# Kernel tuning notes

Hardware: AMD Instinct MI355X
Metric: run time of the kernel (lower is better)

Reference implementation:

```python
import jax, jax.numpy as jnp
from jax import lax
import numpy as np

B, L, C_IN, HID, RANK, NC = 256, 1024, 16, 512, 128, 10
PAD, K = 4, 7  # each conv block: L -> L + 2*PAD - K + 1 = L + 2


def _block(x, dwk, dwb, pwk, pwb, g, b):
    # x: (B, C, L); depthwise conv (groups=C) -> pointwise 1x1 -> batchnorm (batch stats) -> relu
    cin = dwk.shape[0]
    dn = ('NCH', 'OIH', 'NCH')
    y = lax.conv_general_dilated(x, dwk, (1,), [(PAD, PAD)], dimension_numbers=dn,
                                 feature_group_count=cin) + dwb[None, :, None]
    y = lax.conv_general_dilated(y, pwk, (1,), [(0, 0)], dimension_numbers=dn) + pwb[None, :, None]
    m = y.mean(axis=(0, 2), keepdims=True)
    v = y.var(axis=(0, 2), keepdims=True)
    y = (y - m) * lax.rsqrt(v + 1e-5) * g[None, :, None] + b[None, :, None]
    return jax.nn.relu(y)


def _cell(xp, h, c, Ui, Vi, Uh, Vh, bi, bh):
    # low-rank LSTM cell: W = U @ V kept factored for efficiency (same math)
    gates = (xp @ Ui) @ Vi + bi + (h @ Uh) @ Vh + bh  # (B, 4H)
    i, f, g, o = jnp.split(gates, 4, axis=1)
    c = jax.nn.sigmoid(f) * c + jax.nn.sigmoid(i) * jnp.tanh(g)
    h = jax.nn.sigmoid(o) * jnp.tanh(c)
    return h, c


def _forward(x, dw_k1, dw_b1, pw_k1, pw_b1, bn_g1, bn_b1,
             dw_k2, dw_b2, pw_k2, pw_b2, bn_g2, bn_b2,
             dw_k3, dw_b3, pw_k3, pw_b3, bn_g3, bn_b3,
             dw_k4, dw_b4, pw_k4, pw_b4, bn_g4, bn_b4,
             Ui1, Vi1, Uh1, Vh1, bi1, bh1,
             Ui2, Vi2, Uh2, Vh2, bi2, bh2,
             fc_w, fc_b):
    y = x[:, 0].transpose(0, 2, 1)  # (B, C_IN, L)
    y = _block(y, dw_k1, dw_b1, pw_k1, pw_b1, bn_g1, bn_b1)
    y = _block(y, dw_k2, dw_b2, pw_k2, pw_b2, bn_g2, bn_b2)
    y = _block(y, dw_k3, dw_b3, pw_k3, pw_b3, bn_g3, bn_b3)
    y = _block(y, dw_k4, dw_b4, pw_k4, pw_b4, bn_g4, bn_b4)
    # dropout = identity (eval)
    xs = y.transpose(2, 0, 1)  # (T, B, 32), T = L + 8
    bsz = xs.shape[1]
    z = jnp.zeros((bsz, HID), xs.dtype)

    def step(carry, xt):
        h1, c1, h2, c2 = carry
        h1, c1 = _cell(xt, h1, c1, Ui1, Vi1, Uh1, Vh1, bi1, bh1)
        h2, c2 = _cell(h1, h2, c2, Ui2, Vi2, Uh2, Vh2, bi2, bh2)
        return (h1, c1, h2, c2), None

    (h1, c1, h2, c2), _ = lax.scan(step, (z, z, z, z), xs)
    # original stacks all h2 then takes [:, -1, :] -> final h2; dropout = identity
    return h2 @ fc_w.T + fc_b  # (B, NC)


def setup_inputs() -> dict:
    key = jax.random.key(0)
    ks = iter(jax.random.split(key, 64))

    def n(shape, scale=0.05):
        return jax.random.normal(next(ks), shape, jnp.float32) * scale

    inp = {'x': jax.random.normal(next(ks), (B, 1, L, C_IN), jnp.float32)}
    chans = [C_IN, 32, 32, 32]
    for i, cin in enumerate(chans, start=1):
        inp[f'dw_k{i}'] = n((cin, 1, K))
        inp[f'dw_b{i}'] = jnp.zeros((cin,), jnp.float32)
        inp[f'pw_k{i}'] = n((32, cin, 1))
        inp[f'pw_b{i}'] = jnp.zeros((32,), jnp.float32)
        inp[f'bn_g{i}'] = jnp.ones((32,), jnp.float32)
        inp[f'bn_b{i}'] = jnp.zeros((32,), jnp.float32)
    inp['Ui1'] = n((32, RANK)); inp['Vi1'] = n((RANK, 4 * HID))
    inp['Uh1'] = n((HID, RANK)); inp['Vh1'] = n((RANK, 4 * HID))
    inp['bi1'] = jnp.zeros((4 * HID,), jnp.float32); inp['bh1'] = jnp.zeros((4 * HID,), jnp.float32)
    inp['Ui2'] = n((HID, RANK)); inp['Vi2'] = n((RANK, 4 * HID))
    inp['Uh2'] = n((HID, RANK)); inp['Vh2'] = n((RANK, 4 * HID))
    inp['bi2'] = jnp.zeros((4 * HID,), jnp.float32); inp['bh2'] = jnp.zeros((4 * HID,), jnp.float32)
    inp['fc_w'] = n((NC, HID)); inp['fc_b'] = jnp.zeros((NC,), jnp.float32)
    return inp


def reference(x, dw_k1, dw_b1, pw_k1, pw_b1, bn_g1, bn_b1,
              dw_k2, dw_b2, pw_k2, pw_b2, bn_g2, bn_b2,
              dw_k3, dw_b3, pw_k3, pw_b3, bn_g3, bn_b3,
              dw_k4, dw_b4, pw_k4, pw_b4, bn_g4, bn_b4,
              Ui1, Vi1, Uh1, Vh1, bi1, bh1,
              Ui2, Vi2, Uh2, Vh2, bi2, bh2,
              fc_w, fc_b):
    return _forward(x, dw_k1, dw_b1, pw_k1, pw_b1, bn_g1, bn_b1,
                    dw_k2, dw_b2, pw_k2, pw_b2, bn_g2, bn_b2,
                    dw_k3, dw_b3, pw_k3, pw_b3, bn_g3, bn_b3,
                    dw_k4, dw_b4, pw_k4, pw_b4, bn_g4, bn_b4,
                    Ui1, Vi1, Uh1, Vh1, bi1, bh1,
                    Ui2, Vi2, Uh2, Vh2, bi2, bh2,
                    fc_w, fc_b)
```

## Files before the change

### kernel.cpp

```cpp
#include <hip/hip_runtime.h>
#include <stdint.h>
#include <stddef.h>
#include <limits.h>

typedef _Float16 f16;
typedef _Float16 half8 __attribute__((ext_vector_type(8)));
typedef float floatx4 __attribute__((ext_vector_type(4)));
typedef unsigned long long u64;

#define MFMA(a,b,c) __builtin_amdgcn_mfma_f32_16x16x32_f16((a),(b),(c),0,0,0)

static constexpr int LMAX   = 1032;
static constexpr int TSTEPS = 1032;

static constexpr size_t ZBYTES   = (size_t)256*32*LMAX*2;
static constexpr size_t OFF_ZA   = 0;
static constexpr size_t OFF_ZB   = OFF_ZA + ZBYTES;
static constexpr size_t OFF_Y4   = OFF_ZA;
static constexpr size_t OFF_WH1F = OFF_ZB + ZBYTES;
static constexpr size_t OFF_WI2F = OFF_WH1F + (size_t)128*16*64*8*2;
static constexpr size_t OFF_WH2F = OFF_WI2F + (size_t)128*16*64*8*2;
static constexpr size_t OFF_WX1F = OFF_WH2F + (size_t)128*16*64*8*2;
static constexpr size_t OFF_B1   = OFF_WX1F + (size_t)128*64*8*2;
static constexpr size_t OFF_B2   = OFF_B1 + (size_t)2048*4;
static constexpr size_t OFF_STATS= OFF_B2 + (size_t)2048*4;
static constexpr size_t OFF_AB   = OFF_STATS + (size_t)4*64*4;
static constexpr size_t OFF_H1X  = OFF_AB + (size_t)4*64*4;
static constexpr size_t OFF_H2X  = OFF_H1X + (size_t)8*8*32*512*2;
static constexpr size_t OFF_FLAGS= OFF_H2X + (size_t)8*4*32*512*2;

__device__ __forceinline__ float sigm(float x){ return 1.f/(1.f+__expf(-x)); }
__device__ __forceinline__ float tanh_f(float x){ float e=__expf(2.f*x); return (e-1.f)/(e+1.f); }

__device__ __forceinline__ void sta64(void* p, u64 v){
  __hip_atomic_store((u64*)p, v, __ATOMIC_RELAXED, __HIP_MEMORY_SCOPE_AGENT);
}
__device__ __forceinline__ u64 lda64(const void* p){
  return __hip_atomic_load((const u64*)p, __ATOMIC_RELAXED, __HIP_MEMORY_SCOPE_AGENT);
}
__device__ __forceinline__ uint32_t ldf(const uint32_t* p){
  return __hip_atomic_load(p, __ATOMIC_RELAXED, __HIP_MEMORY_SCOPE_AGENT);
}
__device__ __forceinline__ void stf(uint32_t* p, uint32_t v){
  __hip_atomic_store(p, v, __ATOMIC_RELAXED, __HIP_MEMORY_SCOPE_AGENT);
}
__device__ __forceinline__ float4 ldg16(const void* p){
  float4 r;
  asm volatile("global_load_dwordx4 %0, %1, off sc0 sc1" : "=v"(r) : "v"(p) : "memory");
  return r;
}
__device__ __forceinline__ void vmcnt0(){
  asm volatile("s_waitcnt vmcnt(0)" ::: "memory");
}

__device__ __forceinline__ void pollWave(const uint32_t* fl, int t1, int t2){
  const int lane = threadIdx.x & 63;
  int tgt = (lane < 16) ? t1 : ((lane < 32) ? t2 : INT_MIN);
  if (tgt <= 0) tgt = INT_MIN;
  while (true){
    uint32_t v = ldf(&fl[lane & 31]);
    if (__all((int)v >= tgt)) break;
    __builtin_amdgcn_s_sleep(1);
  }
}

__device__ __forceinline__ void stageIssue(float4* r, const f16* src, int tid){
  #pragma unroll
  for (int i=0;i<8;++i){
    int qq = tid + 256*i;
    r[i] = ldg16(src + (size_t)qq*8);
  }
}
__device__ __forceinline__ void stageWrite(uint8_t* base, const float4* r, int tid){
  #pragma unroll
  for (int i=0;i<8;++i){
    int qq = tid + 256*i;
    int row = qq >> 6, ck = qq & 63;
    int cs = ck ^ (row & 15);
    *(float4*)(base + ((row<<6) + cs)*16) = r[i];
  }
}
__device__ __forceinline__ half8 fragLDS(const uint8_t* base, int row, int q, int lq){
  return *(const half8*)(base + (((row<<6)) + (((q<<2)+lq) ^ (row & 15)))*16);
}

__global__ void k_zero(float* stats, uint32_t* flags){
  int bx = blockIdx.x, tid = threadIdx.x;
  if (bx == 4){ if (tid < 256) stats[tid] = 0.f; }
  else flags[bx*256 + tid] = 0u;
}

__global__ __launch_bounds__(256) void k_prep_W(f16* __restrict__ dst, const float* __restrict__ U, const float* __restrict__ V){
  __shared__ float sU[64][65];
  __shared__ float sV[64][68];
  const int tid = threadIdx.x;
  const int n0 = blockIdx.x*64, k0 = blockIdx.y*64;
  const int tx = tid & 15, ty = tid >> 4;
  float acc[4][4];
  #pragma unroll
  for (int a=0;a<4;++a){ acc[a][0]=0.f; acc[a][1]=0.f; acc[a][2]=0.f; acc[a][3]=0.f; }
  for (int rc=0; rc<2; ++rc){
    __syncthreads();
    #pragma unroll
    for (int i=0;i<16;++i){
      int f = tid + 256*i;
      int row = f>>6, col = f&63;
      sU[row][col] = U[(size_t)(k0+row)*128 + rc*64 + col];
      sV[row][col] = V[(size_t)(rc*64+row)*2048 + n0 + col];
    }
    __syncthreads();
    for (int rr=0; rr<64; ++rr){
      float4 bv = *(const float4*)&sV[rr][tx*4];
      #pragma unroll
      for (int a=0;a<4;++a){
        float av = sU[ty*4+a][rr];
        acc[a][0] += av*bv.x; acc[a][1] += av*bv.y; acc[a][2] += av*bv.z; acc[a][3] += av*bv.w;
      }
    }
  }
  #pragma unroll
  for (int a=0;a<4;++a){
    int k = k0 + ty*4 + a;
    int q = k>>5, lq2 = (k>>3)&3, j = k&7;
    #pragma unroll
    for (int c=0;c<4;++c){
      int n = n0 + tx*4 + c;
      int nt = n>>4, lmn = n&15;
      dst[(((size_t)nt*16 + q)*64 + (lq2*16+lmn))*8 + j] = (f16)acc[a][c];
    }
  }
}

__global__ __launch_bounds__(256) void k_prep_Wx(f16* __restrict__ dst, const float* __restrict__ U, const float* __restrict__ V){
  __shared__ float sU[32][129];
  __shared__ float sV[128][68];
  const int tid = threadIdx.x, n0 = blockIdx.x*64;
  for (int f=tid; f<32*128; f+=256) sU[f>>7][f&127] = U[f];
  for (int f=tid; f<128*64; f+=256) sV[f>>6][f&63] = V[(size_t)(f>>6)*2048 + n0 + (f&63)];
  __syncthreads();
  int nn = tid & 63, kb = (tid>>6)*8;
  int n = n0 + nn;
  float acc[8];
  #pragma unroll
  for (int i=0;i<8;++i) acc[i]=0.f;
  for (int r=0;r<128;++r){
    float v = sV[r][nn];
    #pragma unroll
    for (int i=0;i<8;++i) acc[i] += sU[kb+i][r]*v;
  }
  int nt = n>>4, lmn = n&15;
  #pragma unroll
  for (int i=0;i<8;++i){
    int k = kb+i;
    dst[((size_t)nt*64 + (((k>>3)&3)*16 + lmn))*8 + (k&7)] = (f16)acc[i];
  }
}

__global__ void k_prep_bias(float* dst, const float* a, const float* b){
  int idx = blockIdx.x*256 + threadIdx.x;
  if (idx < 2048) dst[idx] = a[idx] + b[idx];
}

__global__ __launch_bounds__(256) void k_conv(
    const float* __restrict__ x0, const f16* __restrict__ zin,
    const float* __restrict__ abp,
    const float* __restrict__ dwk, const float* __restrict__ dwb,
    const float* __restrict__ pwk, const float* __restrict__ pwb,
    f16* __restrict__ zout, float* __restrict__ stats,
    int Lin, int Cin)
{
  const int tid = threadIdx.x;
  const int b = blockIdx.y;
  const int l = blockIdx.x*256 + tid;
  const int Lout = Lin + 2;
  __shared__ float sPw[32*32], sDw[32*7], sDb[32], sPb[32], sAb[64];
  __shared__ float sRed[2][4][32];
  for (int i=tid; i<Cin*32; i+=256) sPw[i] = pwk[i];
  for (int i=tid; i<Cin*7;  i+=256) sDw[i] = dwk[i];
  if (tid < Cin) sDb[tid] = dwb[tid];
  if (tid >= 64 && tid < 96) sPb[tid-64] = pwb[tid-64];
  if (abp != nullptr && tid >= 128 && tid < 192) sAb[tid-128] = abp[tid-128];
  __syncthreads();

  float acc[32];
  #pragma unroll
  for (int o=0;o<32;++o) acc[o] = sPb[o];
  const bool act = (l < Lout);
  if (act){
    for (int c=0;c<Cin;++c){
      float s = sDb[c];
      #pragma unroll
      for (int k=0;k<7;++k){
        int li = l + k - 4;
        float v = 0.f;
        if (li >= 0 && li < Lin){
          if (x0) v = x0[((size_t)b*1024 + li)*16 + c];
          else {
            float z = (float)zin[((size_t)b*32 + c)*LMAX + li];
            v = fmaxf(sAb[c]*z + sAb[32+c], 0.f);
          }
        }
        s += sDw[c*7+k]*v;
      }
      #pragma unroll
      for (int o=0;o<32;++o) acc[o] += sPw[o*Cin + c]*s;
    }
    #pragma unroll
    for (int o=0;o<32;++o) zout[((size_t)b*32 + o)*LMAX + l] = (f16)acc[o];
  }
  const int lane = tid & 63, wv = tid >> 6;
  for (int o=0;o<32;++o){
    float v = act ? acc[o] : 0.f;
    float q = v*v;
    #pragma unroll
    for (int m=1;m<64;m<<=1){ v += __shfl_xor(v,m); q += __shfl_xor(q,m); }
    if (lane == 0){ sRed[0][wv][o] = v; sRed[1][wv][o] = q; }
  }
  __syncthreads();
  if (tid < 32){
    float v = sRed[0][0][tid]+sRed[0][1][tid]+sRed[0][2][tid]+sRed[0][3][tid];
    float q = sRed[1][0][tid]+sRed[1][1][tid]+sRed[1][2][tid]+sRed[1][3][tid];
    atomicAdd(&stats[tid], v);
    atomicAdd(&stats[32+tid], q);
  }
}

__global__ void k_bnfin(const float* __restrict__ stats, const float* __restrict__ g,
                        const float* __restrict__ beta, float* __restrict__ ab, float inv_n)
{
  int o = threadIdx.x;
  if (o < 32){
    float m = stats[o]*inv_n;
    float var = stats[32+o]*inv_n - m*m;
    float a = g[o]*rsqrtf(var + 1e-5f);
    ab[o] = a; ab[32+o] = beta[o] - m*a;
  }
}

__global__ __launch_bounds__(256) void k_y4(const f16* __restrict__ z, const float* __restrict__ ab, f16* __restrict__ y){
  __shared__ f16 sT[32][264];
  __shared__ float sA[64];
  const int b = blockIdx.x, t0 = blockIdx.y*256, tid = threadIdx.x;
  if (tid < 64) sA[tid] = ab[tid];
  __syncthreads();
  #pragma unroll
  for (int i=0;i<8;++i){
    int f = tid + 256*i;
    int ch = f >> 6, tq = f & 63;
    int t = t0 + tq*4;
    if (t < 1032){
      u64 v = *(const u64*)(z + ((size_t)(b*32+ch)*1032 + t));
      union { u64 u; f16 h[4]; } cv; cv.u = v;
      float a = sA[ch], bb = sA[32+ch];
      #pragma unroll
      for (int j=0;j<4;++j) cv.h[j] = (f16)fmaxf(a*(float)cv.h[j] + bb, 0.f);
      *(u64*)&sT[ch][tq*4] = cv.u;
    }
  }
  __syncthreads();
  int t = t0 + tid;
  if (t < 1032){
    union { uint4 v; f16 h[8]; } o[4];
    #pragma unroll
    for (int k=0;k<4;++k)
      #pragma unroll
      for (int j=0;j<8;++j) o[k].h[j] = sT[k*8+j][t - t0];
    uint4* dst = (uint4*)(y + ((size_t)b*1032 + t)*32);
    #pragma unroll
    for (int k=0;k<4;++k) dst[k] = o[k].v;
  }
}

__global__ __launch_bounds__(256,1) void k_lstm(
  const f16* __restrict__ y4x,
  const f16* __restrict__ Wx1F, const f16* __restrict__ Wh1F,
  const f16* __restrict__ Wi2F, const f16* __restrict__ Wh2F,
  const float* __restrict__ bias1, const float* __restrict__ bias2,
  f16* __restrict__ h1x, f16* __restrict__ h2x,
  uint32_t* __restrict__ flags,
  const float* __restrict__ fcw, const float* __restrict__ fcb,
  float* __restrict__ outp)
{
  const int tid  = threadIdx.x;
  const int lane = tid & 63;
  const int w    = tid >> 6;
  const int lm   = lane & 15;
  const int lq   = lane >> 4;
  const int lq8  = lq*8;
  const int g    = blockIdx.x & 7;
  const int idx  = blockIdx.x >> 3;
  const int role = idx >> 4;
  const int b    = idx & 15;

  __shared__ __align__(16) uint8_t bufA[32768];
  __shared__ __align__(16) uint8_t bufB[32768];
  __shared__ float sGate[4*32*33];

  uint32_t* fl = flags + (size_t)g*32;

  const float* biasL = role ? bias2 : bias1;
  float bs[2];
  #pragma unroll
  for (int ct=0; ct<2; ++ct) bs[ct] = biasL[w*512 + b*32 + ct*16 + lm];

  const int nt0 = w*32 + b*2;
  f16* hdst_base = role ? h2x + (size_t)g*4*32*512 : h1x + (size_t)g*8*32*512;

  float creg[4] = {0.f,0.f,0.f,0.f};
  const int cr_row = tid >> 3, cr_u0 = (tid & 7)*4;

  if (role == 0){
    half8 wx[2];
    half8 wB[2][16];
    #pragma unroll
    for (int ct=0; ct<2; ++ct){
      wx[ct] = *(const half8*)&Wx1F[((size_t)(nt0+ct)*64 + lane)*8];
      #pragma unroll
      for (int q=0;q<16;++q)
        wB[ct][q] = *(const half8*)&Wh1F[(((size_t)(nt0+ct)*16 + q)*64 + lane)*8];
    }
    #pragma unroll 1
    for (int t=0; t<TSTEPS; ++t){
      half8 ya0 = *(const half8*)(y4x + ((size_t)(g*32 + lm)*1032 + t)*32 + lq8);
      half8 ya1 = *(const half8*)(y4x + ((size_t)(g*32 + 16 + lm)*1032 + t)*32 + lq8);
      if (w == 0) pollWave(fl, t, t-7);
      __syncthreads();
      float4 st[8];
      if (t >= 1) stageIssue(st, h1x + ((size_t)(g*8 + ((t-1)&7))*32*512), tid);
      floatx4 acc[2][2];
      #pragma unroll
      for (int ct=0; ct<2; ++ct){
        acc[ct][0] = (floatx4){bs[ct],bs[ct],bs[ct],bs[ct]};
        acc[ct][1] = acc[ct][0];
      }
      acc[0][0] = MFMA(ya0, wx[0], acc[0][0]);
      acc[0][1] = MFMA(ya1, wx[0], acc[0][1]);
      acc[1][0] = MFMA(ya0, wx[1], acc[1][0]);
      acc[1][1] = MFMA(ya1, wx[1], acc[1][1]);
      if (t >= 1){
        vmcnt0();
        stageWrite(bufA, st, tid);
      }
      __syncthreads();
      if (t >= 1){
        #pragma unroll
        for (int q=0;q<16;++q){
          half8 a0 = fragLDS(bufA, lm,    q, lq);
          half8 a1 = fragLDS(bufA, 16+lm, q, lq);
          acc[0][0] = MFMA(a0, wB[0][q], acc[0][0]);
          acc[0][1] = MFMA(a1, wB[0][q], acc[0][1]);
          acc[1][0] = MFMA(a0, wB[1][q], acc[1][0]);
          acc[1][1] = MFMA(a1, wB[1][q], acc[1][1]);
        }
      }
      __syncthreads();
      #pragma unroll
      for (int ct=0; ct<2; ++ct)
        #pragma unroll
        for (int rt=0; rt<2; ++rt)
          #pragma unroll
          for (int r=0;r<4;++r)
            sGate[w*1056 + (rt*16 + lq*4 + r)*33 + ct*16 + lm] = acc[ct][rt][r];
      __syncthreads();
      {
        union { u64 uu; f16 h[4]; } hv;
        #pragma unroll
        for (int j=0;j<4;++j){
          int u = cr_u0 + j;
          float iv = sGate[0*1056 + cr_row*33 + u];
          float fv = sGate[1*1056 + cr_row*33 + u];
          float gv = sGate[2*1056 + cr_row*33 + u];
          float ov = sGate[3*1056 + cr_row*33 + u];
          float c = sigm(fv)*creg[j] + sigm(iv)*tanh_f(gv);
          creg[j] = c;
          hv.h[j] = (f16)(sigm(ov)*tanh_f(c));
        }
        f16* dst = hdst_base + (size_t)(t&7)*32*512 + cr_row*512 + b*32 + cr_u0;
        sta64(dst, hv.uu);
      }
      vmcnt0();
      __syncthreads();
      if (tid == 0) stf(&fl[b], (uint32_t)(t+1));
    }
  } else {
    half8 wA[2][16];
    half8 wB[2][16];
    #pragma unroll
    for (int ct=0; ct<2; ++ct)
      #pragma unroll
      for (int q=0;q<16;++q){
        wA[ct][q] = *(const half8*)&Wi2F[(((size_t)(nt0+ct)*16 + q)*64 + lane)*8];
        wB[ct][q] = *(const half8*)&Wh2F[(((size_t)(nt0+ct)*16 + q)*64 + lane)*8];
      }
    #pragma unroll 1
    for (int t=0; t<TSTEPS; ++t){
      if (w == 0) pollWave(fl, t+1, t);
      __syncthreads();
      float4 s0[8], s1[8];
      stageIssue(s0, h1x + ((size_t)(g*8 + (t&7))*32*512), tid);
      if (t >= 1) stageIssue(s1, h2x + ((size_t)(g*4 + ((t-1)&3))*32*512), tid);
      vmcnt0();
      stageWrite(bufA, s0, tid);
      if (t >= 1) stageWrite(bufB, s1, tid);
      __syncthreads();
      floatx4 acc[2][2];
      #pragma unroll
      for (int ct=0; ct<2; ++ct){
        acc[ct][0] = (floatx4){bs[ct],bs[ct],bs[ct],bs[ct]};
        acc[ct][1] = acc[ct][0];
      }
      #pragma unroll
      for (int q=0;q<16;++q){
        half8 a0 = fragLDS(bufA, lm,    q, lq);
        half8 a1 = fragLDS(bufA, 16+lm, q, lq);
        acc[0][0] = MFMA(a0, wA[0][q], acc[0][0]);
        acc[0][1] = MFMA(a1, wA[0][q], acc[0][1]);
        acc[1][0] = MFMA(a0, wA[1][q], acc[1][0]);
        acc[1][1] = MFMA(a1, wA[1][q], acc[1][1]);
      }
      if (t >= 1){
        #pragma unroll
        for (int q=0;q<16;++q){
          half8 a0 = fragLDS(bufB, lm,    q, lq);
          half8 a1 = fragLDS(bufB, 16+lm, q, lq);
          acc[0][0] = MFMA(a0, wB[0][q], acc[0][0]);
          acc[0][1] = MFMA(a1, wB[0][q], acc[0][1]);
          acc[1][0] = MFMA(a0, wB[1][q], acc[1][0]);
          acc[1][1] = MFMA(a1, wB[1][q], acc[1][1]);
        }
      }
      __syncthreads();
      #pragma unroll
      for (int ct=0; ct<2; ++ct)
        #pragma unroll
        for (int rt=0; rt<2; ++rt)
          #pragma unroll
          for (int r=0;r<4;++r)
            sGate[w*1056 + (rt*16 + lq*4 + r)*33 + ct*16 + lm] = acc[ct][rt][r];
      __syncthreads();
      {
        union { u64 uu; f16 h[4]; } hv;
        #pragma unroll
        for (int j=0;j<4;++j){
          int u = cr_u0 + j;
          float iv = sGate[0*1056 + cr_row*33 + u];
          float fv = sGate[1*1056 + cr_row*33 + u];
          float gv = sGate[2*1056 + cr_row*33 + u];
          float ov = sGate[3*1056 + cr_row*33 + u];
          float c = sigm(fv)*creg[j] + sigm(iv)*tanh_f(gv);
          creg[j] = c;
          hv.h[j] = (f16)(sigm(ov)*tanh_f(c));
        }
        f16* dst = hdst_base + (size_t)(t&3)*32*512 + cr_row*512 + b*32 + cr_u0;
        sta64(dst, hv.uu);
      }
      vmcnt0();
      __syncthreads();
      if (tid == 0) stf(&fl[16 + b], (uint32_t)(t+1));
    }
    if (b == 0){
      if (w == 0) pollWave(fl, 0, TSTEPS);
      __syncthreads();
      const f16* hbase = h2x + ((size_t)(g*4 + ((TSTEPS-1)&3))*32*512);
      for (int e = tid; e < 320; e += 256){
        int row = e/10, nc = e%10;
        float s = fcb[nc];
        const float* wv = fcw + (size_t)nc*512;
        const u64* hp = (const u64*)(hbase + row*512);
        for (int k4=0;k4<128;++k4){
          union { u64 uu; f16 h[4]; } cv; cv.uu = lda64(hp + k4);
          #pragma unroll
          for (int i2=0;i2<4;++i2) s += (float)cv.h[i2]*wv[k4*4+i2];
        }
        outp[(size_t)(g*32+row)*10 + nc] = s;
      }
    }
  }
}

extern "C" void kernel_launch(void* const* d_in, const int* in_sizes, int n_in,
                              void* d_out, int out_size, void* d_ws, size_t ws_size,
                              hipStream_t stream)
{
  (void)in_sizes; (void)n_in; (void)out_size; (void)ws_size;
  const float* x = (const float*)d_in[0];
  auto F = [&](int i){ return (const float*)d_in[i]; };
  const float *Ui1=F(25), *Vi1=F(26), *Uh1=F(27), *Vh1=F(28), *bi1=F(29), *bh1=F(30);
  const float *Ui2=F(31), *Vi2=F(32), *Uh2=F(33), *Vh2=F(34), *bi2=F(35), *bh2=F(36);
  const float *fcw=F(37), *fcb=F(38);

  uint8_t* ws = (uint8_t*)d_ws;
  f16* zA   = (f16*)(ws + OFF_ZA);
  f16* zB   = (f16*)(ws + OFF_ZB);
  f16* y4x  = (f16*)(ws + OFF_Y4);
  f16* Wh1F = (f16*)(ws + OFF_WH1F);
  f16* Wi2F = (f16*)(ws + OFF_WI2F);
  f16* Wh2F = (f16*)(ws + OFF_WH2F);
  f16* Wx1F = (f16*)(ws + OFF_WX1F);
  float* bias1 = (float*)(ws + OFF_B1);
  float* bias2 = (float*)(ws + OFF_B2);
  float* stats = (float*)(ws + OFF_STATS);
  float* ab    = (float*)(ws + OFF_AB);
  f16* h1x  = (f16*)(ws + OFF_H1X);
  f16* h2x  = (f16*)(ws + OFF_H2X);
  uint32_t* flags = (uint32_t*)(ws + OFF_FLAGS);
  float* outp = (float*)d_out;

  k_zero<<<5, 256, 0, stream>>>(stats, flags);

  k_prep_W<<<dim3(32,8), 256, 0, stream>>>(Wh1F, Uh1, Vh1);
  k_prep_W<<<dim3(32,8), 256, 0, stream>>>(Wi2F, Ui2, Vi2);
  k_prep_W<<<dim3(32,8), 256, 0, stream>>>(Wh2F, Uh2, Vh2);
  k_prep_Wx<<<32, 256, 0, stream>>>(Wx1F, Ui1, Vi1);
  k_prep_bias<<<8, 256, 0, stream>>>(bias1, bi1, bh1);
  k_prep_bias<<<8, 256, 0, stream>>>(bias2, bi2, bh2);

  dim3 cgrid(5, 256);
  k_conv<<<cgrid, 256, 0, stream>>>(x, nullptr, nullptr, F(1), F(2), F(3), F(4),
                                    zA, stats + 0*64, 1024, 16);
  k_bnfin<<<1, 64, 0, stream>>>(stats + 0*64, F(5), F(6), ab + 0*64, 1.f/(256.f*1026.f));
  k_conv<<<cgrid, 256, 0, stream>>>(nullptr, zA, ab + 0*64, F(7), F(8), F(9), F(10),
                                    zB, stats + 1*64, 1026, 32);
  k_bnfin<<<1, 64, 0, stream>>>(stats + 1*64, F(11), F(12), ab + 1*64, 1.f/(256.f*1028.f));
  k_conv<<<cgrid, 256, 0, stream>>>(nullptr, zB, ab + 1*64, F(13), F(14), F(15), F(16),
                                    zA, stats + 2*64, 1028, 32);
  k_bnfin<<<1, 64, 0, stream>>>(stats + 2*64, F(17), F(18), ab + 2*64, 1.f/(256.f*1030.f));
  k_conv<<<cgrid, 256, 0, stream>>>(nullptr, zA, ab + 2*64, F(19), F(20), F(21), F(22),
                                    zB, stats + 3*64, 1030, 32);
  k_bnfin<<<1, 64, 0, stream>>>(stats + 3*64, F(23), F(24), ab + 3*64, 1.f/(256.f*1032.f));

  k_y4<<<dim3(256,5), 256, 0, stream>>>(zB, ab + 3*64, y4x);

  k_lstm<<<256, 256, 0, stream>>>(y4x,
                                  Wx1F, Wh1F, Wi2F, Wh2F,
                                  bias1, bias2,
                                  h1x, h2x, flags,
                                  fcw, fcb, outp);
}
```

Baseline: 6.313 ms.

## Replace flag-based inter-block sync with timestep-tagged hidden-state words

The LSTM blocks now stop publishing per-step completion flags. Instead, each f16 hidden value is packed into a 32-bit word whose high half carries the timestep, and consumers poll the staged data directly until every tag matches. Layer 2 still publishes a coarse progress counter, which layer 1 checks every four steps to avoid overrunning the ring buffer. This removes the store-drain wait, the extra barriers and the flag polling on the recurrent critical path. The cost is doubled hidden-state traffic and repeated reloads while tags are stale.

```diff
diff --git a/kernel.cpp b/kernel.cpp
--- a/kernel.cpp
+++ b/kernel.cpp
@@ -6,6 +6,7 @@
 typedef _Float16 f16;
 typedef _Float16 half8 __attribute__((ext_vector_type(8)));
 typedef float floatx4 __attribute__((ext_vector_type(4)));
+typedef uint32_t u32x4 __attribute__((ext_vector_type(4)));
 typedef unsigned long long u64;
 
 #define MFMA(a,b,c) __builtin_amdgcn_mfma_f32_16x16x32_f16((a),(b),(c),0,0,0)
@@ -26,68 +27,74 @@
 static constexpr size_t OFF_STATS= OFF_B2 + (size_t)2048*4;
 static constexpr size_t OFF_AB   = OFF_STATS + (size_t)4*64*4;
 static constexpr size_t OFF_H1X  = OFF_AB + (size_t)4*64*4;
-static constexpr size_t OFF_H2X  = OFF_H1X + (size_t)8*8*32*512*2;
-static constexpr size_t OFF_FLAGS= OFF_H2X + (size_t)8*4*32*512*2;
+static constexpr size_t OFF_H2X  = OFF_H1X + (size_t)8*8*32*512*4;
+static constexpr size_t OFF_PROG = OFF_H2X + (size_t)8*4*32*512*4;
 
 __device__ __forceinline__ float sigm(float x){ return 1.f/(1.f+__expf(-x)); }
 __device__ __forceinline__ float tanh_f(float x){ float e=__expf(2.f*x); return (e-1.f)/(e+1.f); }
 
-__device__ __forceinline__ void sta64(void* p, u64 v){
-  __hip_atomic_store((u64*)p, v, __ATOMIC_RELAXED, __HIP_MEMORY_SCOPE_AGENT);
-}
-__device__ __forceinline__ u64 lda64(const void* p){
-  return __hip_atomic_load((const u64*)p, __ATOMIC_RELAXED, __HIP_MEMORY_SCOPE_AGENT);
-}
 __device__ __forceinline__ uint32_t ldf(const uint32_t* p){
   return __hip_atomic_load(p, __ATOMIC_RELAXED, __HIP_MEMORY_SCOPE_AGENT);
 }
 __device__ __forceinline__ void stf(uint32_t* p, uint32_t v){
   __hip_atomic_store(p, v, __ATOMIC_RELAXED, __HIP_MEMORY_SCOPE_AGENT);
 }
-__device__ __forceinline__ float4 ldg16(const void* p){
-  float4 r;
+__device__ __forceinline__ u32x4 ldg16u(const void* p){
+  u32x4 r;
   asm volatile("global_load_dwordx4 %0, %1, off sc0 sc1" : "=v"(r) : "v"(p) : "memory");
   return r;
 }
+__device__ __forceinline__ void stg16(void* p, u32x4 v){
+  asm volatile("global_store_dwordx4 %0, %1, off sc0 sc1" :: "v"(p), "v"(v) : "memory");
+}
 __device__ __forceinline__ void vmcnt0(){
   asm volatile("s_waitcnt vmcnt(0)" ::: "memory");
 }
 
-__device__ __forceinline__ void pollWave(const uint32_t* fl, int t1, int t2){
+__device__ __forceinline__ void pollProg(const uint32_t* pr, int tgt){
   const int lane = threadIdx.x & 63;
-  int tgt = (lane < 16) ? t1 : ((lane < 32) ? t2 : INT_MIN);
-  if (tgt <= 0) tgt = INT_MIN;
   while (true){
-    uint32_t v = ldf(&fl[lane & 31]);
-    if (__all((int)v >= tgt)) break;
+    uint32_t v = (lane < 16) ? ldf(&pr[lane]) : 0x7FFFFFFFu;
+    if (__all(lane >= 16 || (int)v >= tgt)) break;
     __builtin_amdgcn_s_sleep(1);
   }
 }
 
-__device__ __forceinline__ void stageIssue(float4* r, const f16* src, int tid){
-  #pragma unroll
-  for (int i=0;i<8;++i){
-    int qq = tid + 256*i;
-    r[i] = ldg16(src + (size_t)qq*8);
-  }
-}
-__device__ __forceinline__ void stageWrite(uint8_t* base, const float4* r, int tid){
-  #pragma unroll
-  for (int i=0;i<8;++i){
-    int qq = tid + 256*i;
-    int row = qq >> 6, ck = qq & 63;
-    int cs = ck ^ (row & 15);
-    *(float4*)(base + ((row<<6) + cs)*16) = r[i];
+__device__ __forceinline__ void stageTagged(uint8_t* lds, const uint32_t* src, uint32_t tag, int tid){
+  uint32_t pend = 0xFFFFu;
+  u32x4 r[16];
+  while (true){
+    #pragma unroll
+    for (int i=0;i<16;++i)
+      if (pend & (1u<<i)) r[i] = ldg16u(src + (size_t)(tid + 256*i)*4);
+    vmcnt0();
+    #pragma unroll
+    for (int i=0;i<16;++i){
+      if (pend & (1u<<i)){
+        u32x4 v = r[i];
+        if ((v.x>>16)==tag && (v.y>>16)==tag && (v.z>>16)==tag && (v.w>>16)==tag){
+          pend &= ~(1u<<i);
+          int idx = tid + 256*i;
+          int row = idx>>7, c4 = idx&127;
+          int ck = c4>>1, hf = c4&1, cs = ck ^ (row&15);
+          uint32_t lo = (v.x & 0xFFFFu) | (v.y << 16);
+          uint32_t hi = (v.z & 0xFFFFu) | (v.w << 16);
+          *(u64*)(lds + (((row<<6)+cs)<<4) + (hf<<3)) = ((u64)hi<<32) | lo;
+        }
+      }
+    }
+    if (__all(pend == 0)) break;
+    __builtin_amdgcn_s_sleep(1);
   }
 }
 __device__ __forceinline__ half8 fragLDS(const uint8_t* base, int row, int q, int lq){
   return *(const half8*)(base + (((row<<6)) + (((q<<2)+lq) ^ (row & 15)))*16);
 }
 
-__global__ void k_zero(float* stats, uint32_t* flags){
-  int bx = blockIdx.x, tid = threadIdx.x;
-  if (bx == 4){ if (tid < 256) stats[tid] = 0.f; }
-  else flags[bx*256 + tid] = 0u;
+__global__ void k_zero(float* stats, uint32_t* prog){
+  int t = threadIdx.x;
+  stats[t] = 0.f;
+  if (t < 128) prog[t] = 0u;
 }
 
 __global__ __launch_bounds__(256) void k_prep_W(f16* __restrict__ dst, const float* __restrict__ U, const float* __restrict__ V){
@@ -276,8 +283,8 @@
   const f16* __restrict__ Wx1F, const f16* __restrict__ Wh1F,
   const f16* __restrict__ Wi2F, const f16* __restrict__ Wh2F,
   const float* __restrict__ bias1, const float* __restrict__ bias2,
-  f16* __restrict__ h1x, f16* __restrict__ h2x,
-  uint32_t* __restrict__ flags,
+  uint32_t* __restrict__ h1x, uint32_t* __restrict__ h2x,
+  uint32_t* __restrict__ prog,
   const float* __restrict__ fcw, const float* __restrict__ fcb,
   float* __restrict__ outp)
 {
@@ -296,15 +303,15 @@
   __shared__ __align__(16) uint8_t bufB[32768];
   __shared__ float sGate[4*32*33];
 
-  uint32_t* fl = flags + (size_t)g*32;
-
   const float* biasL = role ? bias2 : bias1;
   float bs[2];
   #pragma unroll
   for (int ct=0; ct<2; ++ct) bs[ct] = biasL[w*512 + b*32 + ct*16 + lm];
 
   const int nt0 = w*32 + b*2;
-  f16* hdst_base = role ? h2x + (size_t)g*4*32*512 : h1x + (size_t)g*8*32*512;
+  uint32_t* h1g = h1x + (size_t)g*8*16384;
+  uint32_t* h2g = h2x + (size_t)g*4*16384;
+  uint32_t* prg = prog + (size_t)g*16;
 
   float creg[4] = {0.f,0.f,0.f,0.f};
   const int cr_row = tid >> 3, cr_u0 = (tid & 7)*4;
@@ -323,10 +330,6 @@
     for (int t=0; t<TSTEPS; ++t){
       half8 ya0 = *(const half8*)(y4x + ((size_t)(g*32 + lm)*1032 + t)*32 + lq8);
       half8 ya1 = *(const half8*)(y4x + ((size_t)(g*32 + 16 + lm)*1032 + t)*32 + lq8);
-      if (w == 0) pollWave(fl, t, t-7);
-      __syncthreads();
-      float4 st[8];
-      if (t >= 1) stageIssue(st, h1x + ((size_t)(g*8 + ((t-1)&7))*32*512), tid);
       floatx4 acc[2][2];
       #pragma unroll
       for (int ct=0; ct<2; ++ct){
@@ -337,10 +340,8 @@
       acc[0][1] = MFMA(ya1, wx[0], acc[0][1]);
       acc[1][0] = MFMA(ya0, wx[1], acc[1][0]);
       acc[1][1] = MFMA(ya1, wx[1], acc[1][1]);
-      if (t >= 1){
-        vmcnt0();
-        stageWrite(bufA, st, tid);
-      }
+      if (t >= 1)
+        stageTagged(bufA, h1g + (size_t)((t-1)&7)*16384, (uint32_t)t, tid);
       __syncthreads();
       if (t >= 1){
         #pragma unroll
@@ -361,9 +362,10 @@
           #pragma unroll
           for (int r=0;r<4;++r)
             sGate[w*1056 + (rt*16 + lq*4 + r)*33 + ct*16 + lm] = acc[ct][rt][r];
+      if (w == 0 && t >= 8 && (t & 3) == 0) pollProg(prg, t-3);
       __syncthreads();
       {
-        union { u64 uu; f16 h[4]; } hv;
+        union { uint16_t u[4]; f16 h[4]; } hv;
         #pragma unroll
         for (int j=0;j<4;++j){
           int u = cr_u0 + j;
@@ -375,12 +377,12 @@
           creg[j] = c;
           hv.h[j] = (f16)(sigm(ov)*tanh_f(c));
         }
-        f16* dst = hdst_base + (size_t)(t&7)*32*512 + cr_row*512 + b*32 + cr_u0;
-        sta64(dst, hv.uu);
-      }
-      vmcnt0();
-      __syncthreads();
-      if (tid == 0) stf(&fl[b], (uint32_t)(t+1));
+        uint32_t tg = (uint32_t)(t+1) << 16;
+        u32x4 pv;
+        pv.x = tg | hv.u[0]; pv.y = tg | hv.u[1];
+        pv.z = tg | hv.u[2]; pv.w = tg | hv.u[3];
+        stg16(h1g + (size_t)(t&7)*16384 + cr_row*512 + b*32 + cr_u0, pv);
+      }
     }
   } else {
     half8 wA[2][16];
@@ -394,15 +396,11 @@
       }
     #pragma unroll 1
     for (int t=0; t<TSTEPS; ++t){
-      if (w == 0) pollWave(fl, t+1, t);
-      __syncthreads();
-      float4 s0[8], s1[8];
-      stageIssue(s0, h1x + ((size_t)(g*8 + (t&7))*32*512), tid);
-      if (t >= 1) stageIssue(s1, h2x + ((size_t)(g*4 + ((t-1)&3))*32*512), tid);
-      vmcnt0();
-      stageWrite(bufA, s0, tid);
-      if (t >= 1) stageWrite(bufB, s1, tid);
-      __syncthreads();
+      if (t >= 1)
+        stageTagged(bufB, h2g + (size_t)((t-1)&3)*16384, (uint32_t)t, tid);
+      stageTagged(bufA, h1g + (size_t)(t&7)*16384, (uint32_t)(t+1), tid);
+      __syncthreads();
+      if (tid == 0) stf(&prg[b], (uint32_t)(t+1));
       floatx4 acc[2][2];
       #pragma unroll
       for (int ct=0; ct<2; ++ct){
@@ -439,7 +437,7 @@
             sGate[w*1056 + (rt*16 + lq*4 + r)*33 + ct*16 + lm] = acc[ct][rt][r];
       __syncthreads();
       {
-        union { u64 uu; f16 h[4]; } hv;
+        union { uint16_t u[4]; f16 h[4]; } hv;
         #pragma unroll
         for (int j=0;j<4;++j){
           int u = cr_u0 + j;
@@ -451,26 +449,24 @@
           creg[j] = c;
           hv.h[j] = (f16)(sigm(ov)*tanh_f(c));
         }
-        f16* dst = hdst_base + (size_t)(t&3)*32*512 + cr_row*512 + b*32 + cr_u0;
-        sta64(dst, hv.uu);
-      }
-      vmcnt0();
-      __syncthreads();
-      if (tid == 0) stf(&fl[16 + b], (uint32_t)(t+1));
+        uint32_t tg = (uint32_t)(t+1) << 16;
+        u32x4 pv;
+        pv.x = tg | hv.u[0]; pv.y = tg | hv.u[1];
+        pv.z = tg | hv.u[2]; pv.w = tg | hv.u[3];
+        stg16(h2g + (size_t)(t&3)*16384 + cr_row*512 + b*32 + cr_u0, pv);
+      }
     }
     if (b == 0){
-      if (w == 0) pollWave(fl, 0, TSTEPS);
-      __syncthreads();
-      const f16* hbase = h2x + ((size_t)(g*4 + ((TSTEPS-1)&3))*32*512);
+      stageTagged(bufB, h2g + (size_t)((TSTEPS-1)&3)*16384, (uint32_t)TSTEPS, tid);
+      __syncthreads();
       for (int e = tid; e < 320; e += 256){
         int row = e/10, nc = e%10;
         float s = fcb[nc];
         const float* wv = fcw + (size_t)nc*512;
-        const u64* hp = (const u64*)(hbase + row*512);
-        for (int k4=0;k4<128;++k4){
-          union { u64 uu; f16 h[4]; } cv; cv.uu = lda64(hp + k4);
-          #pragma unroll
-          for (int i2=0;i2<4;++i2) s += (float)cv.h[i2]*wv[k4*4+i2];
+        for (int k=0;k<512;++k){
+          int ck = k>>3, cs = ck ^ (row&15);
+          f16 hvv = *(const f16*)(bufB + (((row<<6)+cs)<<4) + ((k&7)<<1));
+          s += (float)hvv * wv[k];
         }
         outp[(size_t)(g*32+row)*10 + nc] = s;
       }
@@ -501,12 +497,12 @@
   float* bias2 = (float*)(ws + OFF_B2);
   float* stats = (float*)(ws + OFF_STATS);
   float* ab    = (float*)(ws + OFF_AB);
-  f16* h1x  = (f16*)(ws + OFF_H1X);
-  f16* h2x  = (f16*)(ws + OFF_H2X);
-  uint32_t* flags = (uint32_t*)(ws + OFF_FLAGS);
+  uint32_t* h1x = (uint32_t*)(ws + OFF_H1X);
+  uint32_t* h2x = (uint32_t*)(ws + OFF_H2X);
+  uint32_t* prog = (uint32_t*)(ws + OFF_PROG);
   float* outp = (float*)d_out;
 
-  k_zero<<<5, 256, 0, stream>>>(stats, flags);
+  k_zero<<<1, 256, 0, stream>>>(stats, prog);
 
   k_prep_W<<<dim3(32,8), 256, 0, stream>>>(Wh1F, Uh1, Vh1);
   k_prep_W<<<dim3(32,8), 256, 0, stream>>>(Wi2F, Ui2, Vi2);
@@ -534,6 +530,6 @@
   k_lstm<<<256, 256, 0, stream>>>(y4x,
                                   Wx1F, Wh1F, Wi2F, Wh2F,
                                   bias1, bias2,
-                                  h1x, h2x, flags,
+                                  h1x, h2x, prog,
                                   fcw, fcb, outp);
 }
```

After: 10.21 ms. 61.7% more time.
